# Kernel tuning notes

Hardware: AMD Instinct MI355X
Metric: run time of the kernel (lower is better)

Reference implementation:

```python
import jax, jax.numpy as jnp
import numpy as np

B, S, D = 4, 2048, 512
E, K = 8, 2
MH = 4 * D      # resmlp mlp hidden
EH = 2 * D      # expert hidden
EPS = 1e-5


def setup_inputs() -> dict:
    key = jax.random.key(0)
    ks = jax.random.split(key, 16)
    s = 0.02
    return {
        "x": jax.random.normal(ks[0], (B, S, D), dtype=jnp.float32),
        "ln1_g": jnp.ones((D,), jnp.float32), "ln1_b": jnp.zeros((D,), jnp.float32),
        "w1": jax.random.normal(ks[1], (D, MH), jnp.float32) * s,
        "b1": jnp.zeros((MH,), jnp.float32),
        "w2": jax.random.normal(ks[2], (MH, D), jnp.float32) * s,
        "b2": jnp.zeros((D,), jnp.float32),
        "ln2_g": jnp.ones((D,), jnp.float32), "ln2_b": jnp.zeros((D,), jnp.float32),
        "wr": jax.random.normal(ks[3], (E, D), jnp.float32) * s,
        "ew1": jax.random.normal(ks[4], (E, D, EH), jnp.float32) * s,
        "eb1": jnp.zeros((E, EH), jnp.float32),
        "ew2": jax.random.normal(ks[5], (E, EH, D), jnp.float32) * s,
        "eb2": jnp.zeros((E, D), jnp.float32),
        "lnf_g": jnp.ones((D,), jnp.float32), "lnf_b": jnp.zeros((D,), jnp.float32),
    }


def _ln(z, g, b):
    m = z.mean(-1, keepdims=True)
    v = ((z - m) ** 2).mean(-1, keepdims=True)
    return (z - m) * jax.lax.rsqrt(v + EPS) * g + b


def reference(x, ln1_g, ln1_b, w1, b1, w2, b2, ln2_g, ln2_b,
              wr, ew1, eb1, ew2, eb2, lnf_g, lnf_b):
    # ---- ResidualMLPBlock (eval mode: dropout is identity) ----
    h = _ln(x, ln1_g, ln1_b)
    h = jax.nn.gelu(h @ w1 + b1, approximate=False) @ w2 + b2
    x = x + h
    x = _ln(x, ln2_g, ln2_b) + x
    # ---- MoE (eval: no jitter noise, aux_loss = 0) ----
    xf = x.reshape(-1, D)              # [N, D], N = B*S
    n = xf.shape[0]
    probs = jax.nn.softmax(xf @ wr.T, axis=-1)          # [N, E]
    topv, topi = jax.lax.top_k(probs, K)                # [N, K]
    topv = topv / topv.sum(-1, keepdims=True)
    # dense per-token gate per expert: sum over k of renormalized prob where idx==j
    gates = jnp.zeros((n, E), xf.dtype).at[jnp.arange(n)[:, None], topi].add(topv)
    # per-expert MLP over all tokens (masked scatter-combine via gates)
    he = jax.nn.gelu(jnp.einsum("nd,edh->enh", xf, ew1) + eb1[:, None, :],
                     approximate=False)                 # [E, N, 2D]
    ye = jnp.einsum("enh,ehd->end", he, ew2) + eb2[:, None, :]  # [E, N, D]
    out = jnp.einsum("ne,end->nd", gates, ye).reshape(B, S, D)
    # ---- final LayerNorm ----
    out = _ln(out, lnf_g, lnf_b)
    aux_loss = jnp.zeros((), x.dtype)  # eval mode
    return out, aux_loss
```

## Files before the change

kernel.cpp:

```cpp
#include <hip/hip_runtime.h>

#define NTOK 8192
#define DIM  512
#define MHID 2048
#define EHID 1024
#define NEXP 8
#define RBLK 64

using half_t = _Float16;
typedef _Float16 f16x8 __attribute__((ext_vector_type(8)));
typedef float    f32x16 __attribute__((ext_vector_type(16)));

#define MFMA32(a, b, c) __builtin_amdgcn_mfma_f32_32x32x16_f16((a), (b), (c), 0, 0, 0)

typedef const __attribute__((address_space(1))) void* gas_ptr;
typedef __attribute__((address_space(3))) void*       las_ptr;
__device__ __forceinline__ void gl16(const void* g, void* l) {
    __builtin_amdgcn_global_load_lds((gas_ptr)g, (las_ptr)l, 16, 0, 0);
}

__device__ __forceinline__ float gelu_exact(float v) {
    return 0.5f * v * (1.0f + erff(v * 0.70710678118654752f));
}

__device__ __forceinline__ float block_sum4(float v, float* red, int tid) {
#pragma unroll
    for (int off = 32; off; off >>= 1) v += __shfl_down(v, off);
    if ((tid & 63) == 0) red[tid >> 6] = v;
    __syncthreads();
    float r = red[0] + red[1] + red[2] + red[3];
    __syncthreads();
    return r;
}

__global__ __launch_bounds__(256) void ln1_split_kernel(
    const float* __restrict__ x, const float* __restrict__ g, const float* __restrict__ b,
    half_t* __restrict__ xh, half_t* __restrict__ xl, int* __restrict__ cnt)
{
    const int row = blockIdx.x, tid = threadIdx.x;
    if (row == 0) cnt[tid] = 0;
    __shared__ float red[4];
    const size_t base = (size_t)row * DIM;
    float2 v = reinterpret_cast<const float2*>(x + base)[tid];
    float mean = block_sum4(v.x + v.y, red, tid) * (1.0f / DIM);
    float d0 = v.x - mean, d1 = v.y - mean;
    float var = block_sum4(d0 * d0 + d1 * d1, red, tid) * (1.0f / DIM);
    float rstd = rsqrtf(var + 1e-5f);
    int d = tid * 2;
    float y0 = d0 * rstd * g[d]     + b[d];
    float y1 = d1 * rstd * g[d + 1] + b[d + 1];
    half_t h0 = (half_t)y0, h1 = (half_t)y1;
    xh[base + d] = h0;  xh[base + d + 1] = h1;
    xl[base + d]     = (half_t)(y0 - (float)h0);
    xl[base + d + 1] = (half_t)(y1 - (float)h1);
}

__global__ __launch_bounds__(256) void resid_ln2_kernel(
    const float* __restrict__ x, float* __restrict__ p0, const float* __restrict__ p1,
    const float* __restrict__ b2,
    const float* __restrict__ g, const float* __restrict__ b,
    half_t* __restrict__ x3h)
{
    const int row = blockIdx.x, tid = threadIdx.x;
    __shared__ float red[4];
    const size_t base = (size_t)row * DIM;
    float2 xv = reinterpret_cast<const float2*>(x + base)[tid];
    float2 h0 = reinterpret_cast<float2*>(p0 + base)[tid];
    float2 h1 = reinterpret_cast<const float2*>(p1 + base)[tid];
    float2 bb = reinterpret_cast<const float2*>(b2)[tid];
    float z0 = xv.x + h0.x + h1.x + bb.x, z1 = xv.y + h0.y + h1.y + bb.y;
    float mean = block_sum4(z0 + z1, red, tid) * (1.0f / DIM);
    float d0 = z0 - mean, d1 = z1 - mean;
    float var = block_sum4(d0 * d0 + d1 * d1, red, tid) * (1.0f / DIM);
    float rstd = rsqrtf(var + 1e-5f);
    int d = tid * 2;
    float y0 = d0 * rstd * g[d]     + b[d]     + z0;
    float y1 = d1 * rstd * g[d + 1] + b[d + 1] + z1;
    float2 o; o.x = y0; o.y = y1;
    reinterpret_cast<float2*>(p0 + base)[tid] = o;
    x3h[base + d]     = (half_t)y0;
    x3h[base + d + 1] = (half_t)y1;
}

__global__ void transpose_all_kernel(
    const float* __restrict__ w1, const float* __restrict__ w2,
    const float* __restrict__ ew1, const float* __restrict__ ew2,
    half_t* __restrict__ w1t_h, half_t* __restrict__ w1t_l,
    half_t* __restrict__ w2t_h, half_t* __restrict__ w2t_l,
    half_t* __restrict__ ew1t, half_t* __restrict__ ew2t)
{
    int bb = blockIdx.x;
    const float* in; half_t* oh; half_t* ol = (half_t*)0;
    int R, C, cx, cy; size_t mo = 0;
    if (bb < 1024)      { in = w1;  oh = w1t_h; ol = w1t_l; R = 512;  C = 2048; cx = bb & 63; cy = bb >> 6; }
    else if (bb < 2048) { bb -= 1024; in = w2;  oh = w2t_h; ol = w2t_l; R = 2048; C = 512; cx = bb & 15; cy = bb >> 4; }
    else if (bb < 6144) { bb -= 2048; int e = bb >> 9, r = bb & 511;
                          in = ew1; oh = ew1t; R = 512;  C = 1024; mo = (size_t)e * R * C; cx = r & 31; cy = r >> 5; }
    else                { bb -= 6144; int e = bb >> 9, r = bb & 511;
                          in = ew2; oh = ew2t; R = 1024; C = 512;  mo = (size_t)e * R * C; cx = r & 15; cy = r >> 4; }
    __shared__ float t[32][33];
    const int c0 = cx * 32, r0 = cy * 32;
    const int tx = threadIdx.x, ty = threadIdx.y;
    for (int i = ty; i < 32; i += 8) t[i][tx] = in[mo + (size_t)(r0 + i) * C + c0 + tx];
    __syncthreads();
    for (int i = ty; i < 32; i += 8) {
        float v = t[tx][i];
        size_t o = mo + (size_t)(c0 + i) * R + r0 + tx;
        half_t h = (half_t)v;
        oh[o] = h;
        if (ol) ol[o] = (half_t)(v - (float)h);
    }
}

template <int EPI, int NREP>
__global__ __launch_bounds__(512, 2) void gemm8_kernel(
    const half_t* __restrict__ A0, const half_t* __restrict__ A1,
    const half_t* __restrict__ B0, const half_t* __restrict__ B1,
    const float* __restrict__ bias,
    float* __restrict__ Cf0, float* __restrict__ Cf1,
    half_t* __restrict__ Ch, half_t* __restrict__ Cl,
    int Nc, int K, int Ktile)
{
    constexpr int BN    = NREP * 128;
    constexpr int LOADS = 4 + 2 * NREP;
    constexpr int TOT   = 16384 + NREP * 8192;
    __shared__ __align__(16) half_t lds[2 * TOT];

    const int m0 = blockIdx.x * 256, n0 = blockIdx.y * BN;
    const int kbeg = blockIdx.z * Ktile;
    float* Cf = blockIdx.z ? Cf1 : Cf0;
    const int tid = threadIdx.x;
    const int lane = tid & 63, wid = tid >> 6;
    const int wr = wid >> 2, wc = wid & 3;
    const int l31 = lane & 31, l5 = lane >> 5;

    const half_t* gsrc[LOADS];
    {
        const half_t* A0p = A0 + (size_t)m0 * K + kbeg;
        const half_t* A1p = A1 + (size_t)m0 * K + kbeg;
        const half_t* B0p = B0 + (size_t)n0 * K + kbeg;
        const half_t* B1p = B1 + (size_t)n0 * K + kbeg;
#pragma unroll
        for (int i = 0; i < LOADS; i++) {
            int c = tid + 512 * i;
            const half_t* base; int cm;
            if (c < 1024)                  { base = A0p; cm = c; }
            else if (c < 2048)             { base = A1p; cm = c - 1024; }
            else if (c < 2048 + NREP * 512){ base = B0p; cm = c - 2048; }
            else                           { base = B1p; cm = c - 2048 - NREP * 512; }
            int r = cm >> 2, ss = (cm & 3) ^ ((r >> 1) & 3);
            gsrc[i] = base + (size_t)r * K + ss * 8;
        }
    }

    int oa[4][2], ob[NREP][2];
#pragma unroll
    for (int m = 0; m < 4; m++)
#pragma unroll
        for (int kh = 0; kh < 2; kh++) {
            int ra = wr * 128 + m * 32 + l31;
            oa[m][kh] = ra * 32 + (((l5 + 2 * kh) ^ ((ra >> 1) & 3)) << 3);
        }
#pragma unroll
    for (int n = 0; n < NREP; n++)
#pragma unroll
        for (int kh = 0; kh < 2; kh++) {
            int rb = wc * (NREP * 32) + n * 32 + l31;
            ob[n][kh] = rb * 32 + (((l5 + 2 * kh) ^ ((rb >> 1) & 3)) << 3);
        }

    f32x16 acc[4][NREP];
#pragma unroll
    for (int m = 0; m < 4; m++)
#pragma unroll
        for (int n = 0; n < NREP; n++)
#pragma unroll
            for (int q = 0; q < 16; q++) acc[m][n][q] = 0.f;

    auto stage = [&](int bsel, int kof) {
#pragma unroll
        for (int i = 0; i < LOADS; i++)
            gl16(gsrc[i] + kof, &lds[bsel * TOT + (tid + 512 * i) * 8]);
    };
    auto compute = [&](int p) {
        const half_t* buf = &lds[p ? TOT : 0];
        __builtin_amdgcn_s_setprio(1);
#pragma unroll
        for (int kh = 0; kh < 2; kh++) {
            f16x8 ah[4], al[4], bh[NREP], bl[NREP];
#pragma unroll
            for (int m = 0; m < 4; m++) {
                ah[m] = *(const f16x8*)(buf + oa[m][kh]);
                al[m] = *(const f16x8*)(buf + 8192 + oa[m][kh]);
            }
#pragma unroll
            for (int n = 0; n < NREP; n++) {
                bh[n] = *(const f16x8*)(buf + 16384 + ob[n][kh]);
                bl[n] = *(const f16x8*)(buf + 16384 + BN * 32 + ob[n][kh]);
            }
#pragma unroll
            for (int m = 0; m < 4; m++)
#pragma unroll
                for (int n = 0; n < NREP; n++) {
                    acc[m][n] = MFMA32(ah[m], bh[n], acc[m][n]);
                    acc[m][n] = MFMA32(al[m], bh[n], acc[m][n]);
                    acc[m][n] = MFMA32(ah[m], bl[n], acc[m][n]);
                }
        }
        __builtin_amdgcn_s_setprio(0);
    };

    const int nsteps = Ktile / 32;
    stage(0, 0);
#pragma unroll 1
    for (int s = 0; s < nsteps - 1; ++s) {
        stage((s + 1) & 1, (s + 1) * 32);
        if constexpr (NREP == 2) asm volatile("s_waitcnt vmcnt(8)" ::: "memory");
        else                     asm volatile("s_waitcnt vmcnt(6)" ::: "memory");
        __builtin_amdgcn_s_barrier();
        compute(s & 1);
        __builtin_amdgcn_s_barrier();
    }
    asm volatile("s_waitcnt vmcnt(0)" ::: "memory");
    __builtin_amdgcn_s_barrier();
    compute((nsteps - 1) & 1);

    const int er = 4 * l5;
#pragma unroll
    for (int m = 0; m < 4; m++)
#pragma unroll
        for (int n = 0; n < NREP; n++) {
            int cc = n0 + wc * (NREP * 32) + n * 32 + l31;
            float bv = (EPI == 1) ? bias[cc] : 0.f;
#pragma unroll
            for (int reg = 0; reg < 16; reg++) {
                int rr = m0 + wr * 128 + m * 32 + er + 8 * (reg >> 2) + (reg & 3);
                float v = acc[m][n][reg] + bv;
                size_t o = (size_t)rr * Nc + cc;
                if (EPI == 1) {
                    float ge = gelu_exact(v);
                    half_t h = (half_t)ge;
                    Ch[o] = h;
                    Cl[o] = (half_t)(ge - (float)h);
                } else {
                    Cf[o] = v;
                }
            }
        }
}

__global__ __launch_bounds__(256) void router_kernel(
    const float* __restrict__ x3, const float* __restrict__ wrm,
    int* __restrict__ cnt, int* __restrict__ aid, float* __restrict__ gate)
{
    __shared__ float wl[NEXP][DIM];
    __shared__ int   texp[RBLK * 2];
    __shared__ float tgate[RBLK * 2];
    __shared__ int   lslot[RBLK * 2];
    __shared__ int   lcnt[NEXP], lbase[NEXP];
    const int tid = threadIdx.x;
    for (int i = tid; i < NEXP * DIM / 4; i += 256)
        reinterpret_cast<float4*>(&wl[0][0])[i] = reinterpret_cast<const float4*>(wrm)[i];
    if (tid < NEXP) lcnt[tid] = 0;
    __syncthreads();
    const int w = tid >> 6, lane = tid & 63;
#pragma unroll 1
    for (int t = 0; t < RBLK / 4; ++t) {
        const int lt = w * (RBLK / 4) + t;
        const int token = blockIdx.x * RBLK + lt;
        const float* xr = x3 + (size_t)token * DIM;
        float a[NEXP];
#pragma unroll
        for (int e = 0; e < NEXP; e++) a[e] = 0.f;
#pragma unroll
        for (int d0 = 0; d0 < DIM; d0 += 64) {
            float xv = xr[d0 + lane];
#pragma unroll
            for (int e = 0; e < NEXP; e++) a[e] += xv * wl[e][d0 + lane];
        }
#pragma unroll
        for (int e = 0; e < NEXP; e++)
#pragma unroll
            for (int off = 32; off; off >>= 1) a[e] += __shfl_xor(a[e], off);
        if (lane == 0) {
            int i1 = 0; float v1 = a[0];
#pragma unroll
            for (int e = 1; e < NEXP; e++) if (a[e] > v1) { v1 = a[e]; i1 = e; }
            int i2 = -1; float v2 = -3.4e38f;
#pragma unroll
            for (int e = 0; e < NEXP; e++) if (e != i1 && a[e] > v2) { v2 = a[e]; i2 = e; }
            float e2 = expf(v2 - v1);
            float g1 = 1.0f / (1.0f + e2);
            texp[lt * 2]      = i1; tgate[lt * 2]      = g1;
            texp[lt * 2 + 1]  = i2; tgate[lt * 2 + 1]  = 1.0f - g1;
        }
    }
    __syncthreads();
    if (tid < RBLK * 2) lslot[tid] = atomicAdd(&lcnt[texp[tid]], 1);
    __syncthreads();
    if (tid < NEXP) lbase[tid] = atomicAdd(&cnt[tid * 32], lcnt[tid]);
    __syncthreads();
    if (tid < RBLK * 2) {
        const int e = texp[tid];
        const int asg = blockIdx.x * (RBLK * 2) + tid;
        aid[e * NTOK + lbase[e] + lslot[tid]] = asg;
        gate[asg] = tgate[tid];
    }
}

template <int EG, int KDIM, int AROWSHIFT>
__global__ __launch_bounds__(512, 2) void egemm8_kernel(
    const half_t* __restrict__ Ain,
    const half_t* __restrict__ W,
    const float* __restrict__ ebias,
    const int* __restrict__ cnt, const int* __restrict__ aid,
    const float* __restrict__ gate,
    half_t* __restrict__ Oh,
    float* __restrict__ Of,
    int Nc)
{
    const int ntPerE = Nc / 128;
    const int bid = blockIdx.x;
    const int e   = bid / (32 * ntPerE);
    const int rem = bid % (32 * ntPerE);
    const int mt  = rem / ntPerE, nt = rem % ntPerE;
    const int ne  = cnt[e * 32];
    if (mt * 256 >= ne) return;

    constexpr int TOT = 8192 + 4096;
    __shared__ __align__(16) half_t lds[2 * TOT];
    __shared__ int rowmap[256];
    const int tid = threadIdx.x;
    {
        int slot = mt * 256 + tid;
        if (tid < 256) rowmap[tid] = (slot < ne) ? aid[e * NTOK + slot] : -1;
    }
    __syncthreads();

    const int lane = tid & 63, wid = tid >> 6;
    const int wr = wid >> 1, wc = wid & 1;
    const int l31 = lane & 31, l5 = lane >> 5;

    const half_t* gsrc[3];
    const half_t* Wb = W + (size_t)e * Nc * KDIM;
#pragma unroll
    for (int i = 0; i < 3; i++) {
        int c = tid + 512 * i;
        if (c < 1024) {
            int r = c >> 2, ss = (c & 3) ^ ((r >> 1) & 3);
            int a = rowmap[r];
            gsrc[i] = Ain + (size_t)(a >= 0 ? (a >> AROWSHIFT) : 0) * KDIM + ss * 8;
        } else {
            int cb = c - 1024;
            int r = cb >> 2, ss = (cb & 3) ^ ((r >> 1) & 3);
            gsrc[i] = Wb + (size_t)(nt * 128 + r) * KDIM + ss * 8;
        }
    }

    int oa[2][2], ob[2][2];
#pragma unroll
    for (int m = 0; m < 2; m++)
#pragma unroll
        for (int kh = 0; kh < 2; kh++) {
            int ra = wr * 64 + m * 32 + l31;
            oa[m][kh] = ra * 32 + (((l5 + 2 * kh) ^ ((ra >> 1) & 3)) << 3);
        }
#pragma unroll
    for (int n = 0; n < 2; n++)
#pragma unroll
        for (int kh = 0; kh < 2; kh++) {
            int rb = wc * 64 + n * 32 + l31;
            ob[n][kh] = 8192 + rb * 32 + (((l5 + 2 * kh) ^ ((rb >> 1) & 3)) << 3);
        }

    f32x16 acc[2][2];
#pragma unroll
    for (int m = 0; m < 2; m++)
#pragma unroll
        for (int n = 0; n < 2; n++)
#pragma unroll
            for (int q = 0; q < 16; q++) acc[m][n][q] = 0.f;

    auto stage = [&](int bsel, int kof) {
#pragma unroll
        for (int i = 0; i < 3; i++)
            gl16(gsrc[i] + kof, &lds[bsel * TOT + (tid + 512 * i) * 8]);
    };
    auto compute = [&](int p) {
        const half_t* buf = &lds[p ? TOT : 0];
        __builtin_amdgcn_s_setprio(1);
#pragma unroll
        for (int kh = 0; kh < 2; kh++) {
            f16x8 a0 = *(const f16x8*)(buf + oa[0][kh]);
            f16x8 a1 = *(const f16x8*)(buf + oa[1][kh]);
            f16x8 b0 = *(const f16x8*)(buf + ob[0][kh]);
            f16x8 b1 = *(const f16x8*)(buf + ob[1][kh]);
            acc[0][0] = MFMA32(a0, b0, acc[0][0]);
            acc[0][1] = MFMA32(a0, b1, acc[0][1]);
            acc[1][0] = MFMA32(a1, b0, acc[1][0]);
            acc[1][1] = MFMA32(a1, b1, acc[1][1]);
        }
        __builtin_amdgcn_s_setprio(0);
    };

    const int nsteps = KDIM / 32;
    stage(0, 0);
#pragma unroll 1
    for (int s = 0; s < nsteps - 1; ++s) {
        stage((s + 1) & 1, (s + 1) * 32);
        asm volatile("s_waitcnt vmcnt(3)" ::: "memory");
        __builtin_amdgcn_s_barrier();
        compute(s & 1);
        __builtin_amdgcn_s_barrier();
    }
    asm volatile("s_waitcnt vmcnt(0)" ::: "memory");
    __builtin_amdgcn_s_barrier();
    compute((nsteps - 1) & 1);

    const int er = 4 * l5;
#pragma unroll
    for (int m = 0; m < 2; m++)
#pragma unroll
        for (int reg = 0; reg < 16; reg++) {
            int rloc = wr * 64 + m * 32 + er + 8 * (reg >> 2) + (reg & 3);
            int a = rowmap[rloc];
            if (a >= 0) {
#pragma unroll
                for (int n = 0; n < 2; n++) {
                    int cc = nt * 128 + wc * 64 + n * 32 + l31;
                    float v = acc[m][n][reg] + ebias[e * Nc + cc];
                    if (EG == 1) {
                        Oh[(size_t)a * Nc + cc] = (half_t)gelu_exact(v);
                    } else {
                        Of[(size_t)a * Nc + cc] = v * gate[a];
                    }
                }
            }
        }
}

__global__ __launch_bounds__(256) void combine_lnf_kernel(
    const float* __restrict__ Ye, const float* __restrict__ g, const float* __restrict__ b,
    float* __restrict__ out)
{
    const int t = blockIdx.x, tid = threadIdx.x;
    __shared__ float red[4];
    float2 y0 = reinterpret_cast<const float2*>(Ye + (size_t)(2 * t) * DIM)[tid];
    float2 y1 = reinterpret_cast<const float2*>(Ye + (size_t)(2 * t + 1) * DIM)[tid];
    float z0 = y0.x + y1.x, z1 = y0.y + y1.y;
    float mean = block_sum4(z0 + z1, red, tid) * (1.0f / DIM);
    float d0 = z0 - mean, d1 = z1 - mean;
    float var = block_sum4(d0 * d0 + d1 * d1, red, tid) * (1.0f / DIM);
    float rstd = rsqrtf(var + 1e-5f);
    int d = tid * 2;
    out[(size_t)t * DIM + d]     = d0 * rstd * g[d]     + b[d];
    out[(size_t)t * DIM + d + 1] = d1 * rstd * g[d + 1] + b[d + 1];
    if (t == 0 && tid == 0) out[(size_t)NTOK * DIM] = 0.f;
}

extern "C" void kernel_launch(void* const* d_in, const int* in_sizes, int n_in,
                              void* d_out, int out_size, void* d_ws, size_t ws_size,
                              hipStream_t stream)
{
    (void)in_sizes; (void)n_in; (void)out_size; (void)ws_size;
    const float* x    = (const float*)d_in[0];
    const float* ln1g = (const float*)d_in[1];
    const float* ln1b = (const float*)d_in[2];
    const float* w1   = (const float*)d_in[3];
    const float* b1   = (const float*)d_in[4];
    const float* w2   = (const float*)d_in[5];
    const float* b2   = (const float*)d_in[6];
    const float* ln2g = (const float*)d_in[7];
    const float* ln2b = (const float*)d_in[8];
    const float* wrm  = (const float*)d_in[9];
    const float* ew1  = (const float*)d_in[10];
    const float* eb1  = (const float*)d_in[11];
    const float* ew2  = (const float*)d_in[12];
    const float* eb2  = (const float*)d_in[13];
    const float* lnfg = (const float*)d_in[14];
    const float* lnfb = (const float*)d_in[15];
    float* out = (float*)d_out;

    char* w = (char*)d_ws;
    size_t off = 0;
    auto take = [&](size_t bytes) {
        char* p = w + off;
        off += bytes;
        off = (off + 255) & ~(size_t)255;
        return p;
    };
    half_t* xh_h  = (half_t*)take((size_t)NTOK * DIM * 2);
    half_t* xh_l  = (half_t*)take((size_t)NTOK * DIM * 2);
    half_t* w1t_h = (half_t*)take((size_t)DIM * MHID * 2);
    half_t* w1t_l = (half_t*)take((size_t)DIM * MHID * 2);
    half_t* w2t_h = (half_t*)take((size_t)MHID * DIM * 2);
    half_t* w2t_l = (half_t*)take((size_t)MHID * DIM * 2);
    char*   big   = take((size_t)NTOK * MHID * 2 * 2);
    half_t* a1h   = (half_t*)big;
    half_t* a1l   = (half_t*)(big + (size_t)NTOK * MHID * 2);
    half_t* heh   = (half_t*)big;
    float*  yef   = (float*)(big + (size_t)NTOK * MHID * 2);
    float*  x3f   = (float*)take((size_t)NTOK * DIM * 4);
    half_t* x3h   = (half_t*)take((size_t)NTOK * DIM * 2);
    half_t* ew1t  = (half_t*)take((size_t)NEXP * DIM * EHID * 2);
    half_t* ew2t  = (half_t*)take((size_t)NEXP * EHID * DIM * 2);
    int*    cnt   = (int*)take(1024);
    int*    aid   = (int*)take((size_t)NEXP * NTOK * 4);
    float*  gate  = (float*)take((size_t)NTOK * 2 * 4);

    float* p0 = x3f;
    float* p1 = (float*)xh_h;

    ln1_split_kernel<<<NTOK, 256, 0, stream>>>(x, ln1g, ln1b, xh_h, xh_l, cnt);
    transpose_all_kernel<<<10240, dim3(32, 8), 0, stream>>>(
        w1, w2, ew1, ew2, w1t_h, w1t_l, w2t_h, w2t_l, ew1t, ew2t);
    gemm8_kernel<1, 2><<<dim3(NTOK / 256, MHID / 256, 1), 512, 0, stream>>>(
        xh_h, xh_l, w1t_h, w1t_l, b1, (float*)0, (float*)0, a1h, a1l, MHID, DIM, DIM);
    gemm8_kernel<0, 1><<<dim3(NTOK / 256, DIM / 128, 2), 512, 0, stream>>>(
        a1h, a1l, w2t_h, w2t_l, (const float*)0, p0, p1, (half_t*)0, (half_t*)0, DIM, MHID, MHID / 2);
    resid_ln2_kernel<<<NTOK, 256, 0, stream>>>(x, p0, p1, b2, ln2g, ln2b, x3h);
    router_kernel<<<NTOK / RBLK, 256, 0, stream>>>(x3f, wrm, cnt, aid, gate);
    egemm8_kernel<1, DIM, 1><<<NEXP * 32 * (EHID / 128), 512, 0, stream>>>(
        x3h, ew1t, eb1, cnt, aid, (const float*)0, heh, (float*)0, EHID);
    egemm8_kernel<2, EHID, 0><<<NEXP * 32 * (DIM / 128), 512, 0, stream>>>(
        heh, ew2t, eb2, cnt, aid, gate, (half_t*)0, yef, DIM);
    combine_lnf_kernel<<<NTOK, 256, 0, stream>>>(yef, lnfg, lnfb, out);
}
```

Measured before the change: 306.6 us.

## Interleave prefetch with MFMA sub-phases in the first dense GEMM main loop

Adds a FINE variant of the dense GEMM used for the first ResMLP projection (NREP=2). It splits each K-step into four sub-phases, issues the next tile's global-to-LDS loads spread across the first two sub-phases, and brackets each MFMA cluster with barriers, explicit lgkmcnt waits and raised wave priority. The aim is to overlap LDS reads and global loads with matrix math across the two co-resident blocks in a ping-pong style. The cost is many more barriers per K-step and a full vmcnt(0) wait at the start of each step, which could add stalls.

```diff
diff --git a/kernel.cpp b/kernel.cpp
--- a/kernel.cpp
+++ b/kernel.cpp
@@ -112,7 +112,7 @@
     }
 }
 
-template <int EPI, int NREP>
+template <int EPI, int NREP, int FINE>
 __global__ __launch_bounds__(512, 2) void gemm8_kernel(
     const half_t* __restrict__ A0, const half_t* __restrict__ A1,
     const half_t* __restrict__ B0, const half_t* __restrict__ B1,
@@ -182,48 +182,103 @@
         for (int i = 0; i < LOADS; i++)
             gl16(gsrc[i] + kof, &lds[bsel * TOT + (tid + 512 * i) * 8]);
     };
-    auto compute = [&](int p) {
-        const half_t* buf = &lds[p ? TOT : 0];
-        __builtin_amdgcn_s_setprio(1);
-#pragma unroll
-        for (int kh = 0; kh < 2; kh++) {
-            f16x8 ah[4], al[4], bh[NREP], bl[NREP];
-#pragma unroll
-            for (int m = 0; m < 4; m++) {
-                ah[m] = *(const f16x8*)(buf + oa[m][kh]);
-                al[m] = *(const f16x8*)(buf + 8192 + oa[m][kh]);
+
+    const int nsteps = Ktile / 32;
+
+    if constexpr (FINE && NREP == 2) {
+        stage(0, 0);
+#pragma unroll 1
+        for (int s = 0; s < nsteps; ++s) {
+            const half_t* buf = &lds[(s & 1) ? TOT : 0];
+            const int nxt = (s + 1) & 1;
+            const bool more = (s + 1) < nsteps;
+            const int kofn = (s + 1) * 32;
+            asm volatile("s_waitcnt vmcnt(0)" ::: "memory");
+            __builtin_amdgcn_s_barrier();
+            f16x8 bh[2], bl[2];
+#pragma unroll
+            for (int kh = 0; kh < 2; kh++) {
+#pragma unroll
+                for (int mh = 0; mh < 2; mh++) {
+                    if (more && kh == 0) {
+#pragma unroll
+                        for (int i = 0; i < 4; i++) {
+                            int c = mh * 4 + i;
+                            gl16(gsrc[c] + kofn, &lds[nxt * TOT + (tid + 512 * c) * 8]);
+                        }
+                    }
+                    f16x8 ah[2], al[2];
+#pragma unroll
+                    for (int m = 0; m < 2; m++) {
+                        ah[m] = *(const f16x8*)(buf + oa[mh * 2 + m][kh]);
+                        al[m] = *(const f16x8*)(buf + 8192 + oa[mh * 2 + m][kh]);
+                    }
+                    if (mh == 0) {
+#pragma unroll
+                        for (int n = 0; n < 2; n++) {
+                            bh[n] = *(const f16x8*)(buf + 16384 + ob[n][kh]);
+                            bl[n] = *(const f16x8*)(buf + 16384 + BN * 32 + ob[n][kh]);
+                        }
+                    }
+                    __builtin_amdgcn_s_barrier();
+                    asm volatile("s_waitcnt lgkmcnt(0)" ::: "memory");
+                    __builtin_amdgcn_sched_barrier(0);
+                    __builtin_amdgcn_s_setprio(1);
+#pragma unroll
+                    for (int m = 0; m < 2; m++)
+#pragma unroll
+                        for (int n = 0; n < 2; n++) {
+                            acc[mh * 2 + m][n] = MFMA32(ah[m], bh[n], acc[mh * 2 + m][n]);
+                            acc[mh * 2 + m][n] = MFMA32(al[m], bh[n], acc[mh * 2 + m][n]);
+                            acc[mh * 2 + m][n] = MFMA32(ah[m], bl[n], acc[mh * 2 + m][n]);
+                        }
+                    __builtin_amdgcn_s_setprio(0);
+                    __builtin_amdgcn_s_barrier();
+                }
             }
-#pragma unroll
-            for (int n = 0; n < NREP; n++) {
-                bh[n] = *(const f16x8*)(buf + 16384 + ob[n][kh]);
-                bl[n] = *(const f16x8*)(buf + 16384 + BN * 32 + ob[n][kh]);
+        }
+    } else {
+        auto compute = [&](int p) {
+            const half_t* buf = &lds[p ? TOT : 0];
+            __builtin_amdgcn_s_setprio(1);
+#pragma unroll
+            for (int kh = 0; kh < 2; kh++) {
+                f16x8 ah[4], al[4], bh[NREP], bl[NREP];
+#pragma unroll
+                for (int m = 0; m < 4; m++) {
+                    ah[m] = *(const f16x8*)(buf + oa[m][kh]);
+                    al[m] = *(const f16x8*)(buf + 8192 + oa[m][kh]);
+                }
+#pragma unroll
+                for (int n = 0; n < NREP; n++) {
+                    bh[n] = *(const f16x8*)(buf + 16384 + ob[n][kh]);
+                    bl[n] = *(const f16x8*)(buf + 16384 + BN * 32 + ob[n][kh]);
+                }
+#pragma unroll
+                for (int m = 0; m < 4; m++)
+#pragma unroll
+                    for (int n = 0; n < NREP; n++) {
+                        acc[m][n] = MFMA32(ah[m], bh[n], acc[m][n]);
+                        acc[m][n] = MFMA32(al[m], bh[n], acc[m][n]);
+                        acc[m][n] = MFMA32(ah[m], bl[n], acc[m][n]);
+                    }
             }
-#pragma unroll
-            for (int m = 0; m < 4; m++)
-#pragma unroll
-                for (int n = 0; n < NREP; n++) {
-                    acc[m][n] = MFMA32(ah[m], bh[n], acc[m][n]);
-                    acc[m][n] = MFMA32(al[m], bh[n], acc[m][n]);
-                    acc[m][n] = MFMA32(ah[m], bl[n], acc[m][n]);
-                }
-        }
-        __builtin_amdgcn_s_setprio(0);
-    };
-
-    const int nsteps = Ktile / 32;
-    stage(0, 0);
+            __builtin_amdgcn_s_setprio(0);
+        };
+        stage(0, 0);
 #pragma unroll 1
-    for (int s = 0; s < nsteps - 1; ++s) {
-        stage((s + 1) & 1, (s + 1) * 32);
-        if constexpr (NREP == 2) asm volatile("s_waitcnt vmcnt(8)" ::: "memory");
-        else                     asm volatile("s_waitcnt vmcnt(6)" ::: "memory");
+        for (int s = 0; s < nsteps - 1; ++s) {
+            stage((s + 1) & 1, (s + 1) * 32);
+            if constexpr (NREP == 2) asm volatile("s_waitcnt vmcnt(8)" ::: "memory");
+            else                     asm volatile("s_waitcnt vmcnt(6)" ::: "memory");
+            __builtin_amdgcn_s_barrier();
+            compute(s & 1);
+            __builtin_amdgcn_s_barrier();
+        }
+        asm volatile("s_waitcnt vmcnt(0)" ::: "memory");
         __builtin_amdgcn_s_barrier();
-        compute(s & 1);
-        __builtin_amdgcn_s_barrier();
-    }
-    asm volatile("s_waitcnt vmcnt(0)" ::: "memory");
-    __builtin_amdgcn_s_barrier();
-    compute((nsteps - 1) & 1);
+        compute((nsteps - 1) & 1);
+    }
 
     const int er = 4 * l5;
 #pragma unroll
@@ -514,9 +569,9 @@
     ln1_split_kernel<<<NTOK, 256, 0, stream>>>(x, ln1g, ln1b, xh_h, xh_l, cnt);
     transpose_all_kernel<<<10240, dim3(32, 8), 0, stream>>>(
         w1, w2, ew1, ew2, w1t_h, w1t_l, w2t_h, w2t_l, ew1t, ew2t);
-    gemm8_kernel<1, 2><<<dim3(NTOK / 256, MHID / 256, 1), 512, 0, stream>>>(
+    gemm8_kernel<1, 2, 1><<<dim3(NTOK / 256, MHID / 256, 1), 512, 0, stream>>>(
         xh_h, xh_l, w1t_h, w1t_l, b1, (float*)0, (float*)0, a1h, a1l, MHID, DIM, DIM);
-    gemm8_kernel<0, 1><<<dim3(NTOK / 256, DIM / 128, 2), 512, 0, stream>>>(
+    gemm8_kernel<0, 1, 0><<<dim3(NTOK / 256, DIM / 128, 2), 512, 0, stream>>>(
         a1h, a1l, w2t_h, w2t_l, (const float*)0, p0, p1, (half_t*)0, (half_t*)0, DIM, MHID, MHID / 2);
     resid_ln2_kernel<<<NTOK, 256, 0, stream>>>(x, p0, p1, b2, ln2g, ln2b, x3h);
     router_kernel<<<NTOK / RBLK, 256, 0, stream>>>(x3f, wrm, cnt, aid, gate);
```

After: 304.3 us. No clear change (-0.8%).

## Fuse residual+LN2 into router kernel and widen expert GEMM N-tile to 256

Applied to the files above, without the earlier changes.

The residual add and second LayerNorm are merged into the router kernel. Each wavefront normalizes a token in registers, writes the fp16 copy, and computes router logits directly, so the fp32 x3 round trip to memory and one launch go away. Separately, the expert GEMMs now use 256-wide output tiles: four B fragments per wave, twice the LDS B buffer, and half the blocks. This gives more A reuse per loaded row, at the cost of more accumulator registers and LDS, which may lower occupancy.

```diff
diff --git a/kernel.cpp b/kernel.cpp
--- a/kernel.cpp
+++ b/kernel.cpp
@@ -55,33 +55,6 @@
     xl[base + d + 1] = (half_t)(y1 - (float)h1);
 }
 
-__global__ __launch_bounds__(256) void resid_ln2_kernel(
-    const float* __restrict__ x, float* __restrict__ p0, const float* __restrict__ p1,
-    const float* __restrict__ b2,
-    const float* __restrict__ g, const float* __restrict__ b,
-    half_t* __restrict__ x3h)
-{
-    const int row = blockIdx.x, tid = threadIdx.x;
-    __shared__ float red[4];
-    const size_t base = (size_t)row * DIM;
-    float2 xv = reinterpret_cast<const float2*>(x + base)[tid];
-    float2 h0 = reinterpret_cast<float2*>(p0 + base)[tid];
-    float2 h1 = reinterpret_cast<const float2*>(p1 + base)[tid];
-    float2 bb = reinterpret_cast<const float2*>(b2)[tid];
-    float z0 = xv.x + h0.x + h1.x + bb.x, z1 = xv.y + h0.y + h1.y + bb.y;
-    float mean = block_sum4(z0 + z1, red, tid) * (1.0f / DIM);
-    float d0 = z0 - mean, d1 = z1 - mean;
-    float var = block_sum4(d0 * d0 + d1 * d1, red, tid) * (1.0f / DIM);
-    float rstd = rsqrtf(var + 1e-5f);
-    int d = tid * 2;
-    float y0 = d0 * rstd * g[d]     + b[d]     + z0;
-    float y1 = d1 * rstd * g[d + 1] + b[d + 1] + z1;
-    float2 o; o.x = y0; o.y = y1;
-    reinterpret_cast<float2*>(p0 + base)[tid] = o;
-    x3h[base + d]     = (half_t)y0;
-    x3h[base + d + 1] = (half_t)y1;
-}
-
 __global__ void transpose_all_kernel(
     const float* __restrict__ w1, const float* __restrict__ w2,
     const float* __restrict__ ew1, const float* __restrict__ ew2,
@@ -249,8 +222,12 @@
         }
 }
 
-__global__ __launch_bounds__(256) void router_kernel(
-    const float* __restrict__ x3, const float* __restrict__ wrm,
+__global__ __launch_bounds__(256) void resln2_router_kernel(
+    const float* __restrict__ x, const float* __restrict__ p0,
+    const float* __restrict__ p1, const float* __restrict__ b2,
+    const float* __restrict__ g, const float* __restrict__ b,
+    const float* __restrict__ wrm,
+    half_t* __restrict__ x3h,
     int* __restrict__ cnt, int* __restrict__ aid, float* __restrict__ gate)
 {
     __shared__ float wl[NEXP][DIM];
@@ -264,19 +241,57 @@
     if (tid < NEXP) lcnt[tid] = 0;
     __syncthreads();
     const int w = tid >> 6, lane = tid & 63;
+    const int d0 = lane * 8;
+    float wle[NEXP][8];
+#pragma unroll
+    for (int e = 0; e < NEXP; e++)
+#pragma unroll
+        for (int j = 0; j < 8; j++) wle[e][j] = wl[e][d0 + j];
+    float gg[8], bb[8], b2v[8];
+#pragma unroll
+    for (int j = 0; j < 8; j++) { gg[j] = g[d0 + j]; bb[j] = b[d0 + j]; b2v[j] = b2[d0 + j]; }
 #pragma unroll 1
     for (int t = 0; t < RBLK / 4; ++t) {
         const int lt = w * (RBLK / 4) + t;
         const int token = blockIdx.x * RBLK + lt;
-        const float* xr = x3 + (size_t)token * DIM;
+        const size_t base = (size_t)token * DIM + d0;
+        float z[8];
+#pragma unroll
+        for (int h = 0; h < 2; h++) {
+            float4 xa = reinterpret_cast<const float4*>(x + base)[h];
+            float4 pa = reinterpret_cast<const float4*>(p0 + base)[h];
+            float4 qa = reinterpret_cast<const float4*>(p1 + base)[h];
+            z[4 * h + 0] = xa.x + pa.x + qa.x + b2v[4 * h + 0];
+            z[4 * h + 1] = xa.y + pa.y + qa.y + b2v[4 * h + 1];
+            z[4 * h + 2] = xa.z + pa.z + qa.z + b2v[4 * h + 2];
+            z[4 * h + 3] = xa.w + pa.w + qa.w + b2v[4 * h + 3];
+        }
+        float s = 0.f;
+#pragma unroll
+        for (int j = 0; j < 8; j++) s += z[j];
+#pragma unroll
+        for (int off = 32; off; off >>= 1) s += __shfl_xor(s, off);
+        const float mean = s * (1.0f / DIM);
+        float vs = 0.f;
+#pragma unroll
+        for (int j = 0; j < 8; j++) { float d = z[j] - mean; vs += d * d; }
+#pragma unroll
+        for (int off = 32; off; off >>= 1) vs += __shfl_xor(vs, off);
+        const float rstd = rsqrtf(vs * (1.0f / DIM) + 1e-5f);
+        float y[8];
+        f16x8 hv;
+#pragma unroll
+        for (int j = 0; j < 8; j++) {
+            y[j] = (z[j] - mean) * rstd * gg[j] + bb[j] + z[j];
+            hv[j] = (half_t)y[j];
+        }
+        *reinterpret_cast<f16x8*>(x3h + base) = hv;
         float a[NEXP];
 #pragma unroll
-        for (int e = 0; e < NEXP; e++) a[e] = 0.f;
-#pragma unroll
-        for (int d0 = 0; d0 < DIM; d0 += 64) {
-            float xv = xr[d0 + lane];
-#pragma unroll
-            for (int e = 0; e < NEXP; e++) a[e] += xv * wl[e][d0 + lane];
+        for (int e = 0; e < NEXP; e++) {
+            a[e] = 0.f;
+#pragma unroll
+            for (int j = 0; j < 8; j++) a[e] += y[j] * wle[e][j];
         }
 #pragma unroll
         for (int e = 0; e < NEXP; e++)
@@ -291,8 +306,8 @@
             for (int e = 0; e < NEXP; e++) if (e != i1 && a[e] > v2) { v2 = a[e]; i2 = e; }
             float e2 = expf(v2 - v1);
             float g1 = 1.0f / (1.0f + e2);
-            texp[lt * 2]      = i1; tgate[lt * 2]      = g1;
-            texp[lt * 2 + 1]  = i2; tgate[lt * 2 + 1]  = 1.0f - g1;
+            texp[lt * 2]     = i1; tgate[lt * 2]     = g1;
+            texp[lt * 2 + 1] = i2; tgate[lt * 2 + 1] = 1.0f - g1;
         }
     }
     __syncthreads();
@@ -319,7 +334,7 @@
     float* __restrict__ Of,
     int Nc)
 {
-    const int ntPerE = Nc / 128;
+    const int ntPerE = Nc / 256;
     const int bid = blockIdx.x;
     const int e   = bid / (32 * ntPerE);
     const int rem = bid % (32 * ntPerE);
@@ -327,13 +342,13 @@
     const int ne  = cnt[e * 32];
     if (mt * 256 >= ne) return;
 
-    constexpr int TOT = 8192 + 4096;
+    constexpr int TOT = 8192 + 8192;
     __shared__ __align__(16) half_t lds[2 * TOT];
     __shared__ int rowmap[256];
     const int tid = threadIdx.x;
-    {
+    if (tid < 256) {
         int slot = mt * 256 + tid;
-        if (tid < 256) rowmap[tid] = (slot < ne) ? aid[e * NTOK + slot] : -1;
+        rowmap[tid] = (slot < ne) ? aid[e * NTOK + slot] : -1;
     }
     __syncthreads();
 
@@ -341,10 +356,10 @@
     const int wr = wid >> 1, wc = wid & 1;
     const int l31 = lane & 31, l5 = lane >> 5;
 
-    const half_t* gsrc[3];
+    const half_t* gsrc[4];
     const half_t* Wb = W + (size_t)e * Nc * KDIM;
 #pragma unroll
-    for (int i = 0; i < 3; i++) {
+    for (int i = 0; i < 4; i++) {
         int c = tid + 512 * i;
         if (c < 1024) {
             int r = c >> 2, ss = (c & 3) ^ ((r >> 1) & 3);
@@ -353,11 +368,11 @@
         } else {
             int cb = c - 1024;
             int r = cb >> 2, ss = (cb & 3) ^ ((r >> 1) & 3);
-            gsrc[i] = Wb + (size_t)(nt * 128 + r) * KDIM + ss * 8;
-        }
-    }
-
-    int oa[2][2], ob[2][2];
+            gsrc[i] = Wb + (size_t)(nt * 256 + r) * KDIM + ss * 8;
+        }
+    }
+
+    int oa[2][2], ob[4][2];
 #pragma unroll
     for (int m = 0; m < 2; m++)
 #pragma unroll
@@ -366,24 +381,24 @@
             oa[m][kh] = ra * 32 + (((l5 + 2 * kh) ^ ((ra >> 1) & 3)) << 3);
         }
 #pragma unroll
-    for (int n = 0; n < 2; n++)
+    for (int n = 0; n < 4; n++)
 #pragma unroll
         for (int kh = 0; kh < 2; kh++) {
-            int rb = wc * 64 + n * 32 + l31;
+            int rb = wc * 128 + n * 32 + l31;
             ob[n][kh] = 8192 + rb * 32 + (((l5 + 2 * kh) ^ ((rb >> 1) & 3)) << 3);
         }
 
-    f32x16 acc[2][2];
+    f32x16 acc[2][4];
 #pragma unroll
     for (int m = 0; m < 2; m++)
 #pragma unroll
-        for (int n = 0; n < 2; n++)
+        for (int n = 0; n < 4; n++)
 #pragma unroll
             for (int q = 0; q < 16; q++) acc[m][n][q] = 0.f;
 
     auto stage = [&](int bsel, int kof) {
 #pragma unroll
-        for (int i = 0; i < 3; i++)
+        for (int i = 0; i < 4; i++)
             gl16(gsrc[i] + kof, &lds[bsel * TOT + (tid + 512 * i) * 8]);
     };
     auto compute = [&](int p) {
@@ -393,12 +408,14 @@
         for (int kh = 0; kh < 2; kh++) {
             f16x8 a0 = *(const f16x8*)(buf + oa[0][kh]);
             f16x8 a1 = *(const f16x8*)(buf + oa[1][kh]);
-            f16x8 b0 = *(const f16x8*)(buf + ob[0][kh]);
-            f16x8 b1 = *(const f16x8*)(buf + ob[1][kh]);
-            acc[0][0] = MFMA32(a0, b0, acc[0][0]);
-            acc[0][1] = MFMA32(a0, b1, acc[0][1]);
-            acc[1][0] = MFMA32(a1, b0, acc[1][0]);
-            acc[1][1] = MFMA32(a1, b1, acc[1][1]);
+            f16x8 bf[4];
+#pragma unroll
+            for (int n = 0; n < 4; n++) bf[n] = *(const f16x8*)(buf + ob[n][kh]);
+#pragma unroll
+            for (int n = 0; n < 4; n++) {
+                acc[0][n] = MFMA32(a0, bf[n], acc[0][n]);
+                acc[1][n] = MFMA32(a1, bf[n], acc[1][n]);
+            }
         }
         __builtin_amdgcn_s_setprio(0);
     };
@@ -408,7 +425,7 @@
 #pragma unroll 1
     for (int s = 0; s < nsteps - 1; ++s) {
         stage((s + 1) & 1, (s + 1) * 32);
-        asm volatile("s_waitcnt vmcnt(3)" ::: "memory");
+        asm volatile("s_waitcnt vmcnt(4)" ::: "memory");
         __builtin_amdgcn_s_barrier();
         compute(s & 1);
         __builtin_amdgcn_s_barrier();
@@ -426,8 +443,8 @@
             int a = rowmap[rloc];
             if (a >= 0) {
 #pragma unroll
-                for (int n = 0; n < 2; n++) {
-                    int cc = nt * 128 + wc * 64 + n * 32 + l31;
+                for (int n = 0; n < 4; n++) {
+                    int cc = nt * 256 + wc * 128 + n * 32 + l31;
                     float v = acc[m][n][reg] + ebias[e * Nc + cc];
                     if (EG == 1) {
                         Oh[(size_t)a * Nc + cc] = (half_t)gelu_exact(v);
@@ -500,7 +517,7 @@
     half_t* a1l   = (half_t*)(big + (size_t)NTOK * MHID * 2);
     half_t* heh   = (half_t*)big;
     float*  yef   = (float*)(big + (size_t)NTOK * MHID * 2);
-    float*  x3f   = (float*)take((size_t)NTOK * DIM * 4);
+    float*  p0f   = (float*)take((size_t)NTOK * DIM * 4);
     half_t* x3h   = (half_t*)take((size_t)NTOK * DIM * 2);
     half_t* ew1t  = (half_t*)take((size_t)NEXP * DIM * EHID * 2);
     half_t* ew2t  = (half_t*)take((size_t)NEXP * EHID * DIM * 2);
@@ -508,7 +525,7 @@
     int*    aid   = (int*)take((size_t)NEXP * NTOK * 4);
     float*  gate  = (float*)take((size_t)NTOK * 2 * 4);
 
-    float* p0 = x3f;
+    float* p0 = p0f;
     float* p1 = (float*)xh_h;
 
     ln1_split_kernel<<<NTOK, 256, 0, stream>>>(x, ln1g, ln1b, xh_h, xh_l, cnt);
@@ -518,11 +535,11 @@
         xh_h, xh_l, w1t_h, w1t_l, b1, (float*)0, (float*)0, a1h, a1l, MHID, DIM, DIM);
     gemm8_kernel<0, 1><<<dim3(NTOK / 256, DIM / 128, 2), 512, 0, stream>>>(
         a1h, a1l, w2t_h, w2t_l, (const float*)0, p0, p1, (half_t*)0, (half_t*)0, DIM, MHID, MHID / 2);
-    resid_ln2_kernel<<<NTOK, 256, 0, stream>>>(x, p0, p1, b2, ln2g, ln2b, x3h);
-    router_kernel<<<NTOK / RBLK, 256, 0, stream>>>(x3f, wrm, cnt, aid, gate);
-    egemm8_kernel<1, DIM, 1><<<NEXP * 32 * (EHID / 128), 512, 0, stream>>>(
+    resln2_router_kernel<<<NTOK / RBLK, 256, 0, stream>>>(
+        x, p0, p1, b2, ln2g, ln2b, wrm, x3h, cnt, aid, gate);
+    egemm8_kernel<1, DIM, 1><<<NEXP * 32 * (EHID / 256), 512, 0, stream>>>(
         x3h, ew1t, eb1, cnt, aid, (const float*)0, heh, (float*)0, EHID);
-    egemm8_kernel<2, EHID, 0><<<NEXP * 32 * (DIM / 128), 512, 0, stream>>>(
+    egemm8_kernel<2, EHID, 0><<<NEXP * 32 * (DIM / 256), 512, 0, stream>>>(
         heh, ew2t, eb2, cnt, aid, gate, (half_t*)0, yef, DIM);
     combine_lnf_kernel<<<NTOK, 256, 0, stream>>>(yef, lnfg, lnfb, out);
 }
```

Result: slower. 335.9 us (+9.5%).
